# Kernel tuning notes

Hardware: AMD Instinct MI355X
Metric: run time of the kernel (lower is better)

Reference implementation:

```python
import jax, jax.numpy as jnp
import numpy as np

AGENT = 0
TAU = 0.5
EPS = 1e-10


def setup_inputs() -> dict:
    key = jax.random.key(0)
    ks = jax.random.split(key, 8)
    B, A, L, D, AD, OUT = 32768, 6, 225, 128, 64, 5
    E = A - 1  # 5 visible entities
    return {
        "observation": jax.random.normal(ks[0], (B, A, L), dtype=jnp.float32),
        "enc_w": jax.random.normal(ks[1], (L, D), dtype=jnp.float32) * 0.05,
        "enc_b": jnp.zeros((D,), dtype=jnp.float32),
        "q_w": jax.random.normal(ks[2], (D, AD), dtype=jnp.float32) * 0.05,
        "k_w": jax.random.normal(ks[3], (D, AD), dtype=jnp.float32) * 0.05,
        "fc_w": jax.random.normal(ks[4], (2 * E * D, OUT), dtype=jnp.float32) * 0.05,
        "fc_b": jnp.zeros((OUT,), dtype=jnp.float32),
        "u": jax.random.uniform(ks[5], (B, OUT), dtype=jnp.float32),
    }


def reference(observation, enc_w, enc_b, q_w, k_w, fc_w, fc_b, u):
    B, A, L = observation.shape
    others = np.array([i for i in range(A) if i != AGENT])  # static index list
    vis_obs = observation[:, others]          # (B, E, L)
    ag_obs = observation[:, AGENT:AGENT + 1]  # (B, 1, L)

    # ObservationEncoder: Linear + ReLU (shared weights)
    ag_e = jax.nn.relu(ag_obs @ enc_w + enc_b)    # (B, 1, D)
    vis_e = jax.nn.relu(vis_obs @ enc_w + enc_b)  # (B, E, D)

    # EntityAttention: scaled dot-product, softmax over entities
    q = ag_e @ q_w   # (B, 1, AD)
    k = vis_e @ k_w  # (B, E, AD)
    scores = jnp.einsum('bqa,bea->be', q, k) / jnp.sqrt(jnp.asarray(q.shape[-1], q.dtype))
    alphas = jax.nn.softmax(scores, axis=-1)  # (B, E)

    # attention-weighted per-entity encodings
    weighted = alphas[..., None] * vis_e                      # (B, E, D)
    agent_rep = jnp.broadcast_to(ag_e, weighted.shape)        # (B, E, D)
    concat = jnp.concatenate([agent_rep, weighted], axis=-2)  # (B, 2E, D)
    flat = concat.reshape(B, -1)                              # (B, 2*E*D)

    logits = flat @ fc_w + fc_b  # (B, OUT)

    # gumbel_softmax(tau=0.5, hard=False)
    g = -jnp.log(-jnp.log(u + EPS) + EPS)
    probs = jax.nn.softmax((logits + g) / TAU, axis=1)
    predicted_actions = jnp.argmax(probs, axis=1, keepdims=True)  # (B, 1) int
    return predicted_actions
```

## Files before the change

kernel.cpp:

```cpp
#include <hip/hip_runtime.h>
#include <math.h>

#define NB   32768
#define AG   6
#define LL   225
#define DD   128
#define EE   5
#define NOUT 5
#define ADIM 64

#define WS_M        0
#define WS_W1T      16384
#define WS_F2T      17024
#define WS_BSWZ_B   80896

#define SBLK 16
#define NKB  8
#define ENC_STRIDE 132
#define LDS_FLOATS 12672

typedef __attribute__((ext_vector_type(8))) short short8v;
typedef __attribute__((ext_vector_type(4))) float float4v;

__device__ __forceinline__ unsigned short bf_hi(float x, float* rem) {
    unsigned u = __float_as_uint(x);
    unsigned r = (u + 0x7FFFu + ((u >> 16) & 1u)) & 0xFFFF0000u;
    *rem = x - __uint_as_float(r);
    return (unsigned short)(r >> 16);
}

__device__ __forceinline__ int aslot(int kbL, int mt, int s, int la) {
    return ((((kbL * 6 + mt) * 3 + s) * 64) + la) * 8;
}

__global__ void precompute_kernel(const float* __restrict__ q_w,
                                  const float* __restrict__ k_w,
                                  const float* __restrict__ enc_w,
                                  const float* __restrict__ fc_w,
                                  float* __restrict__ ws) {
    int b = blockIdx.x;
    int t = threadIdx.x;
    if (b < 128) {
        float s = 0.f;
        #pragma unroll 8
        for (int j = 0; j < ADIM; ++j)
            s = fmaf(q_w[b * ADIM + j], k_w[t * ADIM + j], s);
        ws[WS_M + b * 128 + t] = s * 0.125f;
    } else if (b == 128) {
        int d = t;
        #pragma unroll
        for (int o = 0; o < NOUT; ++o) {
            float s = 0.f;
            #pragma unroll
            for (int e = 0; e < EE; ++e)
                s += fc_w[(e * 128 + d) * NOUT + o];
            ws[WS_W1T + o * 128 + d] = s;
            #pragma unroll
            for (int e = 0; e < EE; ++e)
                ws[WS_F2T + (e * 5 + o) * 128 + d] = fc_w[(640 + e * 128 + d) * NOUT + o];
        }
    } else {
        int idx = (b - 129) * 128 + t;
        int lane = idx & 63;
        int rest = idx >> 6;
        int s    = rest % 3;
        int r2   = rest / 3;
        int nt   = r2 & 7;
        int kb   = r2 >> 3;
        unsigned short* bs = (unsigned short*)((char*)ws + WS_BSWZ_B);
        const int n     = nt * 16 + (lane & 15);
        const int kbase = kb * 32 + (lane >> 4) * 8;
        #pragma unroll
        for (int j = 0; j < 8; ++j) {
            int k = kbase + j;
            float x = (k < LL) ? enc_w[k * DD + n] : 0.f;
            float q1, q2, q3;
            unsigned short h = bf_hi(x,  &q1);
            unsigned short m = bf_hi(q1, &q2);
            unsigned short l = bf_hi(q2, &q3);
            bs[(((kb * 8 + nt) * 3 + s) * 64 + lane) * 8 + j] =
                (s == 0) ? h : (s == 1) ? m : l;
        }
    }
}

__global__ __launch_bounds__(256, 2)
void policy_kernel(const float* __restrict__ obs,
                   const float* __restrict__ enc_b,
                   const float* __restrict__ fc_b,
                   const float* __restrict__ u,
                   const float* __restrict__ ws,
                   int* __restrict__ out) {
    __shared__ float lds[LDS_FLOATS];
    unsigned short* aswz = (unsigned short*)lds;

    const int tid  = threadIdx.x;
    const int lane = tid & 63;
    const int w    = tid >> 6;
    const int bs0  = blockIdx.x * SBLK;
    const float* obs_blk = obs + (size_t)bs0 * (AG * LL);
    const unsigned short* bswz = (const unsigned short*)((const char*)ws + WS_BSWZ_B);

    float4v acc[6][2];
    #pragma unroll
    for (int mt = 0; mt < 6; ++mt)
        #pragma unroll
        for (int nt = 0; nt < 2; ++nt)
            acc[mt][nt] = (float4v){0.f, 0.f, 0.f, 0.f};

    #pragma unroll 1
    for (int c = 0; c < 4; ++c) {
        const int k0 = 64 * c;
        #pragma unroll
        for (int rr = 0; rr < 6; ++rr) {
            const int r  = rr * 16 + (tid >> 4);
            const int k4 = tid & 15;
            const int k  = k0 + 4 * k4;
            float4 v = make_float4(0.f, 0.f, 0.f, 0.f);
            if (k + 3 <= 224)      v = *(const float4*)&obs_blk[r * LL + k];
            else if (k == 224)     v.x = obs_blk[r * LL + 224];
            float vf[4] = {v.x, v.y, v.z, v.w};
            unsigned long long ph = 0, pm = 0, pl = 0;
            #pragma unroll
            for (int e = 0; e < 4; ++e) {
                float q1, q2, q3;
                unsigned short h = bf_hi(vf[e], &q1);
                unsigned short m = bf_hi(q1,    &q2);
                unsigned short l = bf_hi(q2,    &q3);
                ph |= (unsigned long long)h << (16 * e);
                pm |= (unsigned long long)m << (16 * e);
                pl |= (unsigned long long)l << (16 * e);
            }
            const int mt  = r >> 4, mm = r & 15;
            const int kbL = k4 >> 3;
            const int kk  = (4 * k4) & 31;
            const int la  = mm + 16 * (kk >> 3);
            const int j0  = kk & 7;
            *(unsigned long long*)&aswz[aslot(kbL, mt, 0, la) + j0] = ph;
            *(unsigned long long*)&aswz[aslot(kbL, mt, 1, la) + j0] = pm;
            *(unsigned long long*)&aswz[aslot(kbL, mt, 2, la) + j0] = pl;
        }
        __syncthreads();

        #pragma unroll
        for (int kbL = 0; kbL < 2; ++kbL) {
            const int kb = 2 * c + kbL;
            short8v Bf[2][3];
            #pragma unroll
            for (int nt = 0; nt < 2; ++nt)
                #pragma unroll
                for (int s = 0; s < 3; ++s)
                    Bf[nt][s] = *(const short8v*)
                        &bswz[(((kb * 8 + (2 * w + nt)) * 3 + s) * 64 + lane) * 8];
            #pragma unroll
            for (int mt = 0; mt < 6; ++mt) {
                short8v Ah = *(const short8v*)&aswz[aslot(kbL, mt, 0, lane)];
                short8v Am = *(const short8v*)&aswz[aslot(kbL, mt, 1, lane)];
                short8v Al = *(const short8v*)&aswz[aslot(kbL, mt, 2, lane)];
                #pragma unroll
                for (int nt = 0; nt < 2; ++nt) {
                    float4v d = acc[mt][nt];
                    d = __builtin_amdgcn_mfma_f32_16x16x32_bf16(Ah, Bf[nt][0], d, 0, 0, 0);
                    d = __builtin_amdgcn_mfma_f32_16x16x32_bf16(Ah, Bf[nt][1], d, 0, 0, 0);
                    d = __builtin_amdgcn_mfma_f32_16x16x32_bf16(Am, Bf[nt][0], d, 0, 0, 0);
                    d = __builtin_amdgcn_mfma_f32_16x16x32_bf16(Ah, Bf[nt][2], d, 0, 0, 0);
                    d = __builtin_amdgcn_mfma_f32_16x16x32_bf16(Al, Bf[nt][0], d, 0, 0, 0);
                    d = __builtin_amdgcn_mfma_f32_16x16x32_bf16(Am, Bf[nt][1], d, 0, 0, 0);
                    acc[mt][nt] = d;
                }
            }
        }
        __syncthreads();
    }

    {
        #pragma unroll
        for (int nt = 0; nt < 2; ++nt) {
            const int col = (2 * w + nt) * 16 + (lane & 15);
            const float bb = enc_b[col];
            #pragma unroll
            for (int mt = 0; mt < 6; ++mt) {
                const int rbase = mt * 16 + (lane >> 4) * 4;
                #pragma unroll
                for (int reg = 0; reg < 4; ++reg)
                    lds[(rbase + reg) * ENC_STRIDE + col] =
                        fmaxf(acc[mt][nt][reg] + bb, 0.f);
            }
        }
    }
    __syncthreads();

    const float* Mw = ws + WS_M;
    const int c0 = 2 * lane;

    #pragma unroll 1
    for (int p = 0; p < 2; ++p) {
        const int sA = 4 * w + 2 * p;
        const int rA = sA * AG;
        const int rB = (sA + 1) * AG;

        float t0[2] = {0.f, 0.f}, t1[2] = {0.f, 0.f};
        #pragma unroll 4
        for (int d = 0; d < DD; d += 4) {
            float4 a0 = *(const float4*)&lds[rA * ENC_STRIDE + d];
            float4 a1 = *(const float4*)&lds[rB * ENC_STRIDE + d];
            float2 m0 = *(const float2*)&Mw[(size_t)(d + 0) * DD + c0];
            float2 m1 = *(const float2*)&Mw[(size_t)(d + 1) * DD + c0];
            float2 m2 = *(const float2*)&Mw[(size_t)(d + 2) * DD + c0];
            float2 m3 = *(const float2*)&Mw[(size_t)(d + 3) * DD + c0];
            t0[0] = fmaf(a0.x, m0.x, t0[0]); t1[0] = fmaf(a0.x, m0.y, t1[0]);
            t0[0] = fmaf(a0.y, m1.x, t0[0]); t1[0] = fmaf(a0.y, m1.y, t1[0]);
            t0[0] = fmaf(a0.z, m2.x, t0[0]); t1[0] = fmaf(a0.z, m2.y, t1[0]);
            t0[0] = fmaf(a0.w, m3.x, t0[0]); t1[0] = fmaf(a0.w, m3.y, t1[0]);
            t0[1] = fmaf(a1.x, m0.x, t0[1]); t1[1] = fmaf(a1.x, m0.y, t1[1]);
            t0[1] = fmaf(a1.y, m1.x, t0[1]); t1[1] = fmaf(a1.y, m1.y, t1[1]);
            t0[1] = fmaf(a1.z, m2.x, t0[1]); t1[1] = fmaf(a1.z, m2.y, t1[1]);
            t0[1] = fmaf(a1.w, m3.x, t0[1]); t1[1] = fmaf(a1.w, m3.y, t1[1]);
        }

        float vx[2][EE], vy[2][EE], sc[2][EE];
        #pragma unroll
        for (int j = 0; j < 2; ++j)
            #pragma unroll
            for (int e = 0; e < EE; ++e) {
                float2 v = *(const float2*)&lds[((sA + j) * AG + 1 + e) * ENC_STRIDE + c0];
                vx[j][e] = v.x; vy[j][e] = v.y;
                sc[j][e] = t0[j] * v.x + t1[j] * v.y;
            }
        #pragma unroll
        for (int off = 32; off > 0; off >>= 1)
            #pragma unroll
            for (int j = 0; j < 2; ++j)
                #pragma unroll
                for (int e = 0; e < EE; ++e)
                    sc[j][e] += __shfl_xor(sc[j][e], off, 64);

        float alpha[2][EE];
        #pragma unroll
        for (int j = 0; j < 2; ++j) {
            float mx = sc[j][0];
            #pragma unroll
            for (int e = 1; e < EE; ++e) mx = fmaxf(mx, sc[j][e]);
            float sum = 0.f;
            #pragma unroll
            for (int e = 0; e < EE; ++e) { alpha[j][e] = expf(sc[j][e] - mx); sum += alpha[j][e]; }
            const float inv = 1.f / sum;
            #pragma unroll
            for (int e = 0; e < EE; ++e) alpha[j][e] *= inv;
        }

        float Lg[2][NOUT];
        #pragma unroll
        for (int j = 0; j < 2; ++j) {
            float2 a2 = *(const float2*)&lds[(sA + j) * AG * ENC_STRIDE + c0];
            #pragma unroll
            for (int o = 0; o < NOUT; ++o) {
                float2 w1 = *(const float2*)&ws[WS_W1T + o * DD + c0];
                Lg[j][o] = fmaf(a2.x, w1.x, a2.y * w1.y);
            }
        }
        #pragma unroll
        for (int e = 0; e < EE; ++e) {
            float wxj[2], wyj[2];
            #pragma unroll
            for (int j = 0; j < 2; ++j) { wxj[j] = alpha[j][e] * vx[j][e]; wyj[j] = alpha[j][e] * vy[j][e]; }
            #pragma unroll
            for (int o = 0; o < NOUT; ++o) {
                float2 f2 = *(const float2*)&ws[WS_F2T + (e * NOUT + o) * DD + c0];
                #pragma unroll
                for (int j = 0; j < 2; ++j)
                    Lg[j][o] = fmaf(wxj[j], f2.x, fmaf(wyj[j], f2.y, Lg[j][o]));
            }
        }
        #pragma unroll
        for (int off = 32; off > 0; off >>= 1)
            #pragma unroll
            for (int j = 0; j < 2; ++j)
                #pragma unroll
                for (int o = 0; o < NOUT; ++o)
                    Lg[j][o] += __shfl_xor(Lg[j][o], off, 64);

        const int S0 = bs0 + sA;
        float y = -1e30f;
        if (lane < 10) {
            const int jl = lane / 5, ol = lane - 5 * jl;
            const float uu  = u[(size_t)S0 * NOUT + lane];
            const float gmb = -logf(-logf(uu + 1e-10f) + 1e-10f);
            y = Lg[jl][ol] + fc_b[ol] + gmb;
        }
        float b0 = -1e30f, b1 = -1e30f; int bi0 = 0, bi1 = 0;
        #pragma unroll
        for (int o = 0; o < NOUT; ++o) {
            float y0 = __shfl(y, o, 64);
            float y1 = __shfl(y, 5 + o, 64);
            if (y0 > b0) { b0 = y0; bi0 = o; }
            if (y1 > b1) { b1 = y1; bi1 = o; }
        }
        if (lane < 2) out[S0 + lane] = lane ? bi1 : bi0;
    }
}

extern "C" void kernel_launch(void* const* d_in, const int* in_sizes, int n_in,
                              void* d_out, int out_size, void* d_ws, size_t ws_size,
                              hipStream_t stream) {
    const float* obs   = (const float*)d_in[0];
    const float* enc_w = (const float*)d_in[1];
    const float* enc_b = (const float*)d_in[2];
    const float* q_w   = (const float*)d_in[3];
    const float* k_w   = (const float*)d_in[4];
    const float* fc_w  = (const float*)d_in[5];
    const float* fc_b  = (const float*)d_in[6];
    const float* uu    = (const float*)d_in[7];
    float* ws = (float*)d_ws;
    int*   po = (int*)d_out;

    precompute_kernel<<<225, 128, 0, stream>>>(q_w, k_w, enc_w, fc_w, ws);
    policy_kernel<<<NB / SBLK, 256, 0, stream>>>(obs, enc_b, fc_b, uu, ws, po);
}
```

Baseline: 402.3 us.

## Use 512-thread blocks with 2D warp tiling, swizzled LDS, and truncating bf16 split

The block doubles to 512 threads (8 warps). Warps are arranged 2x4 over row and column tiles, so each warp keeps 3x2 accumulators instead of 6x2, and the attention/logit tail runs without its two-pass loop. Observation staging now loads 8 floats per thread, splits them into bf16 hi/mid/lo with perm-based truncation instead of round-to-nearest, and writes 128-bit stores into an XOR-swizzled LDS layout to reduce bank conflicts. The aim is more waves per CU to hide global-load latency and less staging cost. In exchange, the B fragments are re-read by more warps, and the truncating split may change rounding slightly.

```diff
diff --git a/kernel.cpp b/kernel.cpp
--- a/kernel.cpp
+++ b/kernel.cpp
@@ -15,7 +15,6 @@
 #define WS_BSWZ_B   80896
 
 #define SBLK 16
-#define NKB  8
 #define ENC_STRIDE 132
 #define LDS_FLOATS 12672
 
@@ -29,8 +28,46 @@
     return (unsigned short)(r >> 16);
 }
 
-__device__ __forceinline__ int aslot(int kbL, int mt, int s, int la) {
-    return ((((kbL * 6 + mt) * 3 + s) * 64) + la) * 8;
+struct Tri { unsigned h, m, l; };
+__device__ __forceinline__ Tri split2(float x0, float x1) {
+    Tri t;
+    unsigned u0 = __float_as_uint(x0), u1 = __float_as_uint(x1);
+    t.h = __builtin_amdgcn_perm(u1, u0, 0x07060302u);
+    float r0 = x0 - __uint_as_float(u0 & 0xFFFF0000u);
+    float r1 = x1 - __uint_as_float(u1 & 0xFFFF0000u);
+    unsigned v0 = __float_as_uint(r0), v1 = __float_as_uint(r1);
+    t.m = __builtin_amdgcn_perm(v1, v0, 0x07060302u);
+    float q0 = r0 - __uint_as_float(v0 & 0xFFFF0000u);
+    float q1 = r1 - __uint_as_float(v1 & 0xFFFF0000u);
+    t.l = __builtin_amdgcn_perm(__float_as_uint(q1), __float_as_uint(q0), 0x07060302u);
+    return t;
+}
+
+__device__ __forceinline__ void stage8(unsigned short* aswz, const float* obs_blk,
+                                       int slot, int k0) {
+    const int r  = slot >> 3;
+    const int k8 = slot & 7;
+    const int k  = k0 + 8 * k8;
+    float4 v0 = make_float4(0.f, 0.f, 0.f, 0.f);
+    float4 v1 = make_float4(0.f, 0.f, 0.f, 0.f);
+    if (k + 7 <= 224) {
+        v0 = *(const float4*)&obs_blk[r * LL + k];
+        v1 = *(const float4*)&obs_blk[r * LL + k + 4];
+    } else if (k == 224) {
+        v0.x = obs_blk[r * LL + 224];
+    }
+    Tri a = split2(v0.x, v0.y);
+    Tri b = split2(v0.z, v0.w);
+    Tri cc = split2(v1.x, v1.y);
+    Tri d = split2(v1.z, v1.w);
+    const int mt  = r >> 4, mm = r & 15;
+    const int kbL = k8 >> 2;
+    const int la  = mm + 16 * (k8 & 3);
+    const int pla = la ^ ((la >> 2) & 12);
+    unsigned short* p = aswz + ((kbL * 6 + mt) * 3) * 512 + pla * 8;
+    *(uint4*)(p)        = make_uint4(a.h, b.h, cc.h, d.h);
+    *(uint4*)(p + 512)  = make_uint4(a.m, b.m, cc.m, d.m);
+    *(uint4*)(p + 1024) = make_uint4(a.l, b.l, cc.l, d.l);
 }
 
 __global__ void precompute_kernel(const float* __restrict__ q_w,
@@ -84,7 +121,7 @@
     }
 }
 
-__global__ __launch_bounds__(256, 2)
+__global__ __launch_bounds__(512, 4)
 void policy_kernel(const float* __restrict__ obs,
                    const float* __restrict__ enc_b,
                    const float* __restrict__ fc_b,
@@ -97,49 +134,25 @@
     const int tid  = threadIdx.x;
     const int lane = tid & 63;
     const int w    = tid >> 6;
+    const int wr   = w >> 2;
+    const int wc   = w & 3;
     const int bs0  = blockIdx.x * SBLK;
     const float* obs_blk = obs + (size_t)bs0 * (AG * LL);
     const unsigned short* bswz = (const unsigned short*)((const char*)ws + WS_BSWZ_B);
-
-    float4v acc[6][2];
-    #pragma unroll
-    for (int mt = 0; mt < 6; ++mt)
+    const int pl8 = (lane ^ ((lane >> 2) & 12)) * 8;
+
+    float4v acc[3][2];
+    #pragma unroll
+    for (int m3 = 0; m3 < 3; ++m3)
         #pragma unroll
         for (int nt = 0; nt < 2; ++nt)
-            acc[mt][nt] = (float4v){0.f, 0.f, 0.f, 0.f};
+            acc[m3][nt] = (float4v){0.f, 0.f, 0.f, 0.f};
 
     #pragma unroll 1
     for (int c = 0; c < 4; ++c) {
         const int k0 = 64 * c;
-        #pragma unroll
-        for (int rr = 0; rr < 6; ++rr) {
-            const int r  = rr * 16 + (tid >> 4);
-            const int k4 = tid & 15;
-            const int k  = k0 + 4 * k4;
-            float4 v = make_float4(0.f, 0.f, 0.f, 0.f);
-            if (k + 3 <= 224)      v = *(const float4*)&obs_blk[r * LL + k];
-            else if (k == 224)     v.x = obs_blk[r * LL + 224];
-            float vf[4] = {v.x, v.y, v.z, v.w};
-            unsigned long long ph = 0, pm = 0, pl = 0;
-            #pragma unroll
-            for (int e = 0; e < 4; ++e) {
-                float q1, q2, q3;
-                unsigned short h = bf_hi(vf[e], &q1);
-                unsigned short m = bf_hi(q1,    &q2);
-                unsigned short l = bf_hi(q2,    &q3);
-                ph |= (unsigned long long)h << (16 * e);
-                pm |= (unsigned long long)m << (16 * e);
-                pl |= (unsigned long long)l << (16 * e);
-            }
-            const int mt  = r >> 4, mm = r & 15;
-            const int kbL = k4 >> 3;
-            const int kk  = (4 * k4) & 31;
-            const int la  = mm + 16 * (kk >> 3);
-            const int j0  = kk & 7;
-            *(unsigned long long*)&aswz[aslot(kbL, mt, 0, la) + j0] = ph;
-            *(unsigned long long*)&aswz[aslot(kbL, mt, 1, la) + j0] = pm;
-            *(unsigned long long*)&aswz[aslot(kbL, mt, 2, la) + j0] = pl;
-        }
+        stage8(aswz, obs_blk, tid, k0);
+        if (tid < 256) stage8(aswz, obs_blk, 512 + tid, k0);
         __syncthreads();
 
         #pragma unroll
@@ -151,22 +164,24 @@
                 #pragma unroll
                 for (int s = 0; s < 3; ++s)
                     Bf[nt][s] = *(const short8v*)
-                        &bswz[(((kb * 8 + (2 * w + nt)) * 3 + s) * 64 + lane) * 8];
-            #pragma unroll
-            for (int mt = 0; mt < 6; ++mt) {
-                short8v Ah = *(const short8v*)&aswz[aslot(kbL, mt, 0, lane)];
-                short8v Am = *(const short8v*)&aswz[aslot(kbL, mt, 1, lane)];
-                short8v Al = *(const short8v*)&aswz[aslot(kbL, mt, 2, lane)];
+                        &bswz[(((kb * 8 + (2 * wc + nt)) * 3 + s) * 64 + lane) * 8];
+            #pragma unroll
+            for (int m3 = 0; m3 < 3; ++m3) {
+                const unsigned short* ap =
+                    aswz + ((kbL * 6 + (wr * 3 + m3)) * 3) * 512 + pl8;
+                short8v Ah = *(const short8v*)(ap);
+                short8v Am = *(const short8v*)(ap + 512);
+                short8v Al = *(const short8v*)(ap + 1024);
                 #pragma unroll
                 for (int nt = 0; nt < 2; ++nt) {
-                    float4v d = acc[mt][nt];
+                    float4v d = acc[m3][nt];
                     d = __builtin_amdgcn_mfma_f32_16x16x32_bf16(Ah, Bf[nt][0], d, 0, 0, 0);
                     d = __builtin_amdgcn_mfma_f32_16x16x32_bf16(Ah, Bf[nt][1], d, 0, 0, 0);
                     d = __builtin_amdgcn_mfma_f32_16x16x32_bf16(Am, Bf[nt][0], d, 0, 0, 0);
                     d = __builtin_amdgcn_mfma_f32_16x16x32_bf16(Ah, Bf[nt][2], d, 0, 0, 0);
                     d = __builtin_amdgcn_mfma_f32_16x16x32_bf16(Al, Bf[nt][0], d, 0, 0, 0);
                     d = __builtin_amdgcn_mfma_f32_16x16x32_bf16(Am, Bf[nt][1], d, 0, 0, 0);
-                    acc[mt][nt] = d;
+                    acc[m3][nt] = d;
                 }
             }
         }
@@ -176,15 +191,15 @@
     {
         #pragma unroll
         for (int nt = 0; nt < 2; ++nt) {
-            const int col = (2 * w + nt) * 16 + (lane & 15);
+            const int col = (2 * wc + nt) * 16 + (lane & 15);
             const float bb = enc_b[col];
             #pragma unroll
-            for (int mt = 0; mt < 6; ++mt) {
-                const int rbase = mt * 16 + (lane >> 4) * 4;
+            for (int m3 = 0; m3 < 3; ++m3) {
+                const int rbase = (wr * 3 + m3) * 16 + (lane >> 4) * 4;
                 #pragma unroll
                 for (int reg = 0; reg < 4; ++reg)
                     lds[(rbase + reg) * ENC_STRIDE + col] =
-                        fmaxf(acc[mt][nt][reg] + bb, 0.f);
+                        fmaxf(acc[m3][nt][reg] + bb, 0.f);
             }
         }
     }
@@ -192,112 +207,108 @@
 
     const float* Mw = ws + WS_M;
     const int c0 = 2 * lane;
-
-    #pragma unroll 1
-    for (int p = 0; p < 2; ++p) {
-        const int sA = 4 * w + 2 * p;
-        const int rA = sA * AG;
-        const int rB = (sA + 1) * AG;
-
-        float t0[2] = {0.f, 0.f}, t1[2] = {0.f, 0.f};
-        #pragma unroll 4
-        for (int d = 0; d < DD; d += 4) {
-            float4 a0 = *(const float4*)&lds[rA * ENC_STRIDE + d];
-            float4 a1 = *(const float4*)&lds[rB * ENC_STRIDE + d];
-            float2 m0 = *(const float2*)&Mw[(size_t)(d + 0) * DD + c0];
-            float2 m1 = *(const float2*)&Mw[(size_t)(d + 1) * DD + c0];
-            float2 m2 = *(const float2*)&Mw[(size_t)(d + 2) * DD + c0];
-            float2 m3 = *(const float2*)&Mw[(size_t)(d + 3) * DD + c0];
-            t0[0] = fmaf(a0.x, m0.x, t0[0]); t1[0] = fmaf(a0.x, m0.y, t1[0]);
-            t0[0] = fmaf(a0.y, m1.x, t0[0]); t1[0] = fmaf(a0.y, m1.y, t1[0]);
-            t0[0] = fmaf(a0.z, m2.x, t0[0]); t1[0] = fmaf(a0.z, m2.y, t1[0]);
-            t0[0] = fmaf(a0.w, m3.x, t0[0]); t1[0] = fmaf(a0.w, m3.y, t1[0]);
-            t0[1] = fmaf(a1.x, m0.x, t0[1]); t1[1] = fmaf(a1.x, m0.y, t1[1]);
-            t0[1] = fmaf(a1.y, m1.x, t0[1]); t1[1] = fmaf(a1.y, m1.y, t1[1]);
-            t0[1] = fmaf(a1.z, m2.x, t0[1]); t1[1] = fmaf(a1.z, m2.y, t1[1]);
-            t0[1] = fmaf(a1.w, m3.x, t0[1]); t1[1] = fmaf(a1.w, m3.y, t1[1]);
-        }
-
-        float vx[2][EE], vy[2][EE], sc[2][EE];
+    const int sA = 2 * w;
+    const int rA = sA * AG;
+    const int rB = rA + AG;
+
+    float t0[2] = {0.f, 0.f}, t1[2] = {0.f, 0.f};
+    #pragma unroll 4
+    for (int d = 0; d < DD; d += 4) {
+        float4 a0 = *(const float4*)&lds[rA * ENC_STRIDE + d];
+        float4 a1 = *(const float4*)&lds[rB * ENC_STRIDE + d];
+        float2 m0 = *(const float2*)&Mw[(size_t)(d + 0) * DD + c0];
+        float2 m1 = *(const float2*)&Mw[(size_t)(d + 1) * DD + c0];
+        float2 m2 = *(const float2*)&Mw[(size_t)(d + 2) * DD + c0];
+        float2 m3 = *(const float2*)&Mw[(size_t)(d + 3) * DD + c0];
+        t0[0] = fmaf(a0.x, m0.x, t0[0]); t1[0] = fmaf(a0.x, m0.y, t1[0]);
+        t0[0] = fmaf(a0.y, m1.x, t0[0]); t1[0] = fmaf(a0.y, m1.y, t1[0]);
+        t0[0] = fmaf(a0.z, m2.x, t0[0]); t1[0] = fmaf(a0.z, m2.y, t1[0]);
+        t0[0] = fmaf(a0.w, m3.x, t0[0]); t1[0] = fmaf(a0.w, m3.y, t1[0]);
+        t0[1] = fmaf(a1.x, m0.x, t0[1]); t1[1] = fmaf(a1.x, m0.y, t1[1]);
+        t0[1] = fmaf(a1.y, m1.x, t0[1]); t1[1] = fmaf(a1.y, m1.y, t1[1]);
+        t0[1] = fmaf(a1.z, m2.x, t0[1]); t1[1] = fmaf(a1.z, m2.y, t1[1]);
+        t0[1] = fmaf(a1.w, m3.x, t0[1]); t1[1] = fmaf(a1.w, m3.y, t1[1]);
+    }
+
+    float vx[2][EE], vy[2][EE], sc[2][EE];
+    #pragma unroll
+    for (int j = 0; j < 2; ++j)
+        #pragma unroll
+        for (int e = 0; e < EE; ++e) {
+            float2 v = *(const float2*)&lds[((sA + j) * AG + 1 + e) * ENC_STRIDE + c0];
+            vx[j][e] = v.x; vy[j][e] = v.y;
+            sc[j][e] = t0[j] * v.x + t1[j] * v.y;
+        }
+    #pragma unroll
+    for (int off = 32; off > 0; off >>= 1)
         #pragma unroll
         for (int j = 0; j < 2; ++j)
             #pragma unroll
-            for (int e = 0; e < EE; ++e) {
-                float2 v = *(const float2*)&lds[((sA + j) * AG + 1 + e) * ENC_STRIDE + c0];
-                vx[j][e] = v.x; vy[j][e] = v.y;
-                sc[j][e] = t0[j] * v.x + t1[j] * v.y;
-            }
-        #pragma unroll
-        for (int off = 32; off > 0; off >>= 1)
+            for (int e = 0; e < EE; ++e)
+                sc[j][e] += __shfl_xor(sc[j][e], off, 64);
+
+    float alpha[2][EE];
+    #pragma unroll
+    for (int j = 0; j < 2; ++j) {
+        float mx = sc[j][0];
+        #pragma unroll
+        for (int e = 1; e < EE; ++e) mx = fmaxf(mx, sc[j][e]);
+        float sum = 0.f;
+        #pragma unroll
+        for (int e = 0; e < EE; ++e) { alpha[j][e] = expf(sc[j][e] - mx); sum += alpha[j][e]; }
+        const float inv = 1.f / sum;
+        #pragma unroll
+        for (int e = 0; e < EE; ++e) alpha[j][e] *= inv;
+    }
+
+    float Lg[2][NOUT];
+    #pragma unroll
+    for (int j = 0; j < 2; ++j) {
+        float2 a2 = *(const float2*)&lds[(sA + j) * AG * ENC_STRIDE + c0];
+        #pragma unroll
+        for (int o = 0; o < NOUT; ++o) {
+            float2 w1 = *(const float2*)&ws[WS_W1T + o * DD + c0];
+            Lg[j][o] = fmaf(a2.x, w1.x, a2.y * w1.y);
+        }
+    }
+    #pragma unroll
+    for (int e = 0; e < EE; ++e) {
+        float wxj[2], wyj[2];
+        #pragma unroll
+        for (int j = 0; j < 2; ++j) { wxj[j] = alpha[j][e] * vx[j][e]; wyj[j] = alpha[j][e] * vy[j][e]; }
+        #pragma unroll
+        for (int o = 0; o < NOUT; ++o) {
+            float2 f2 = *(const float2*)&ws[WS_F2T + (e * NOUT + o) * DD + c0];
             #pragma unroll
             for (int j = 0; j < 2; ++j)
-                #pragma unroll
-                for (int e = 0; e < EE; ++e)
-                    sc[j][e] += __shfl_xor(sc[j][e], off, 64);
-
-        float alpha[2][EE];
-        #pragma unroll
-        for (int j = 0; j < 2; ++j) {
-            float mx = sc[j][0];
-            #pragma unroll
-            for (int e = 1; e < EE; ++e) mx = fmaxf(mx, sc[j][e]);
-            float sum = 0.f;
-            #pragma unroll
-            for (int e = 0; e < EE; ++e) { alpha[j][e] = expf(sc[j][e] - mx); sum += alpha[j][e]; }
-            const float inv = 1.f / sum;
-            #pragma unroll
-            for (int e = 0; e < EE; ++e) alpha[j][e] *= inv;
-        }
-
-        float Lg[2][NOUT];
-        #pragma unroll
-        for (int j = 0; j < 2; ++j) {
-            float2 a2 = *(const float2*)&lds[(sA + j) * AG * ENC_STRIDE + c0];
-            #pragma unroll
-            for (int o = 0; o < NOUT; ++o) {
-                float2 w1 = *(const float2*)&ws[WS_W1T + o * DD + c0];
-                Lg[j][o] = fmaf(a2.x, w1.x, a2.y * w1.y);
-            }
-        }
-        #pragma unroll
-        for (int e = 0; e < EE; ++e) {
-            float wxj[2], wyj[2];
-            #pragma unroll
-            for (int j = 0; j < 2; ++j) { wxj[j] = alpha[j][e] * vx[j][e]; wyj[j] = alpha[j][e] * vy[j][e]; }
-            #pragma unroll
-            for (int o = 0; o < NOUT; ++o) {
-                float2 f2 = *(const float2*)&ws[WS_F2T + (e * NOUT + o) * DD + c0];
-                #pragma unroll
-                for (int j = 0; j < 2; ++j)
-                    Lg[j][o] = fmaf(wxj[j], f2.x, fmaf(wyj[j], f2.y, Lg[j][o]));
-            }
-        }
-        #pragma unroll
-        for (int off = 32; off > 0; off >>= 1)
-            #pragma unroll
-            for (int j = 0; j < 2; ++j)
-                #pragma unroll
-                for (int o = 0; o < NOUT; ++o)
-                    Lg[j][o] += __shfl_xor(Lg[j][o], off, 64);
-
-        const int S0 = bs0 + sA;
-        float y = -1e30f;
-        if (lane < 10) {
-            const int jl = lane / 5, ol = lane - 5 * jl;
-            const float uu  = u[(size_t)S0 * NOUT + lane];
-            const float gmb = -logf(-logf(uu + 1e-10f) + 1e-10f);
-            y = Lg[jl][ol] + fc_b[ol] + gmb;
-        }
-        float b0 = -1e30f, b1 = -1e30f; int bi0 = 0, bi1 = 0;
-        #pragma unroll
-        for (int o = 0; o < NOUT; ++o) {
-            float y0 = __shfl(y, o, 64);
-            float y1 = __shfl(y, 5 + o, 64);
-            if (y0 > b0) { b0 = y0; bi0 = o; }
-            if (y1 > b1) { b1 = y1; bi1 = o; }
-        }
-        if (lane < 2) out[S0 + lane] = lane ? bi1 : bi0;
-    }
+                Lg[j][o] = fmaf(wxj[j], f2.x, fmaf(wyj[j], f2.y, Lg[j][o]));
+        }
+    }
+    #pragma unroll
+    for (int off = 32; off > 0; off >>= 1)
+        #pragma unroll
+        for (int j = 0; j < 2; ++j)
+            #pragma unroll
+            for (int o = 0; o < NOUT; ++o)
+                Lg[j][o] += __shfl_xor(Lg[j][o], off, 64);
+
+    const int S0 = bs0 + sA;
+    float y = -1e30f;
+    if (lane < 10) {
+        const int jl = lane / 5, ol = lane - 5 * jl;
+        const float uu  = u[(size_t)S0 * NOUT + lane];
+        const float gmb = -logf(-logf(uu + 1e-10f) + 1e-10f);
+        y = Lg[jl][ol] + fc_b[ol] + gmb;
+    }
+    float b0 = -1e30f, b1 = -1e30f; int bi0 = 0, bi1 = 0;
+    #pragma unroll
+    for (int o = 0; o < NOUT; ++o) {
+        float y0 = __shfl(y, o, 64);
+        float y1 = __shfl(y, 5 + o, 64);
+        if (y0 > b0) { b0 = y0; bi0 = o; }
+        if (y1 > b1) { b1 = y1; bi1 = o; }
+    }
+    if (lane < 2) out[S0 + lane] = lane ? bi1 : bi0;
 }
 
 extern "C" void kernel_launch(void* const* d_in, const int* in_sizes, int n_in,
@@ -315,5 +326,5 @@
     int*   po = (int*)d_out;
 
     precompute_kernel<<<225, 128, 0, stream>>>(q_w, k_w, enc_w, fc_w, ws);
-    policy_kernel<<<NB / SBLK, 256, 0, stream>>>(obs, enc_b, fc_b, uu, ws, po);
-}
+    policy_kernel<<<NB / SBLK, 512, 0, stream>>>(obs, enc_b, fc_b, uu, ws, po);
+}
```

Result: faster. 366.7 us (-8.9%).
